# Kernel optimization log

Measured on AMD Instinct MI355X. Metric: run time of the kernel, lower is better.

The kernel has to match this reference:

```python
import jax, jax.numpy as jnp
import numpy as np

B, N, D = 8, 2048, 192
G, S = 512, 32
OUT = 384
ALPHA, BETA = 1000.0, 100.0
EPS = 1e-05


def setup_inputs() -> dict:
    key = jax.random.key(0)
    ks = jax.random.split(key, 8)
    sc = 0.02
    return {
        "points": jax.random.normal(ks[0], (B, N, 3), jnp.float32),
        "feats": jax.random.normal(ks[1], (B, N, D), jnp.float32),
        # 1x1 conv weights (BN assumed folded, inference form)
        "W1": sc * jax.random.normal(ks[2], (OUT, 2 * D), jnp.float32),
        "b1": jnp.zeros((OUT,), jnp.float32),
        "Wa": sc * jax.random.normal(ks[3], (OUT // 2, OUT), jnp.float32),
        "ba": jnp.zeros((OUT // 2,), jnp.float32),
        "Wb": sc * jax.random.normal(ks[4], (OUT, OUT // 2), jnp.float32),
        "bb": jnp.zeros((OUT,), jnp.float32),
    }


def fps(pts, n_samples):
    """Farthest point sampling. pts: (B,N,3) -> idx (B,n_samples) int32."""
    def one(p):  # (N,3)
        def step(carry, _):
            dists, last = carry
            cur = p[last]                                 # (3,)
            d = jnp.sum((p - cur) ** 2, axis=-1)          # (N,)
            dists = jnp.minimum(dists, d)
            nxt = jnp.argmax(dists).astype(jnp.int32)
            return (dists, nxt), last
        init = (jnp.full((p.shape[0],), jnp.inf, p.dtype), jnp.int32(0))
        _, idxs = jax.lax.scan(step, init, None, length=n_samples)
        return idxs
    return jax.vmap(one)(pts)


def pairwise_sqdist(a, b):
    # a: (B,G,3), b: (B,N,3) -> (B,G,N)
    aa = jnp.sum(a * a, -1)[:, :, None]
    bb = jnp.sum(b * b, -1)[:, None, :]
    return aa + bb - 2.0 * jnp.einsum('bgd,bnd->bgn', a, b)


def group_points(x, idx):
    # x: (B,N,C), idx: (B,G,S) -> (B,G,S,C)
    return jax.vmap(lambda f, i: f[i])(x, idx)


def pos_embed(xyz):
    # xyz: (B,G,S,3) -> (B,G,S,OUT)  Fourier positional encoding
    in_dim = xyz.shape[-1]
    feat_dim = OUT // (2 * in_dim)
    freq = jnp.arange(feat_dim, dtype=xyz.dtype)
    denom = jnp.power(jnp.asarray(ALPHA, xyz.dtype), freq / feat_dim)
    z = BETA * xyz[..., None] / denom                      # (B,G,S,3,feat_dim)
    pos = jnp.concatenate([jnp.sin(z), jnp.cos(z)], axis=-1)
    return pos.reshape(*xyz.shape[:-1], OUT)


def _forward(points, feats, W1, b1, Wa, ba, Wb, bb):
    # FPS centers
    fps_idx = fps(points, G)                               # (B,G)
    centers = jax.vmap(lambda p, i: p[i])(points, fps_idx)  # (B,G,3)

    d2 = pairwise_sqdist(centers, points)                  # (B,G,N)
    _, knn_idx = jax.lax.top_k(-d2, S)                     # (B,G,S)

    neighbor_pts = group_points(points, knn_idx)           # (B,G,S,3)
    neighbor_feats = group_points(feats, knn_idx)          # (B,G,S,D)

    # 'sim' normalization: global (scalar, unbiased) std of centered neighbors
    diff = neighbor_pts - centers[:, :, None, :]
    m = jnp.mean(diff)
    std = jnp.sqrt(jnp.sum((diff - m) ** 2) / (diff.size - 1))
    neighbor_pts = diff / (std + EPS)

    # center feats via 1-NN of centers in points
    center_idx = jnp.argmin(d2, axis=-1)                   # (B,G)
    center_feats = jax.vmap(lambda f, i: f[i])(feats, center_idx)  # (B,G,D)

    # concat neighbor + broadcast center feats -> (B,G,S,2D)
    gf = jnp.concatenate(
        [neighbor_feats, jnp.broadcast_to(center_feats[:, :, None, :], (points.shape[0], G, S, D))],
        axis=-1)

    # shared MLP (1x1 conv) + ReLU
    gf = jax.nn.relu(jnp.einsum('bgsc,oc->bgso', gf, W1) + b1)  # (B,G,S,OUT)

    pos = pos_embed(neighbor_pts)                          # (B,G,S,OUT)
    gf = (gf + pos) * pos

    # residual block: conv(OUT->OUT/2)+ReLU, conv(OUT/2->OUT), +x, ReLU
    h = jax.nn.relu(jnp.einsum('bgso,ho->bgsh', gf, Wa) + ba)
    h = jnp.einsum('bgsh,oh->bgso', h, Wb) + bb
    gf = jax.nn.relu(h + gf)

    # fused max + mean pooling over neighbors (S)
    out = jnp.max(gf, axis=2) + jnp.mean(gf, axis=2)       # (B,G,OUT)
    return centers, out


def reference(points, feats, W1, b1, Wa, ba, Wb, bb):
    return _forward(points, feats, W1, b1, Wa, ba, Wb, bb)
```

## Files before the change

kernel.cpp:

```cpp
#include <hip/hip_runtime.h>
#include <math.h>

#define Bn   8
#define Nn   2048
#define Dn   192
#define Gn   512
#define Sn   32
#define OUTn 384
#define Mrows (Bn * Gn * Sn)

typedef __attribute__((ext_vector_type(8))) unsigned short ushortx8;
typedef __attribute__((ext_vector_type(8))) __bf16 bf16x8;
typedef __attribute__((ext_vector_type(4))) float floatx4;

static constexpr size_t OFF_KNN   = 0;
static constexpr size_t OFF_CIDX  = 524288;
static constexpr size_t OFF_DIFF  = 540672;
static constexpr size_t OFF_SUMS  = 2113536;
static constexpr size_t OFF_STD   = 2113552;
static constexpr size_t OFF_DENOM = 2113792;
static constexpr size_t OFF_W1B   = 2114048;
static constexpr size_t OFF_WAB   = 2408960;
static constexpr size_t OFF_WBB   = 2556416;
static constexpr size_t OFF_G1    = 2703872;
static constexpr size_t OFF_FEATB = 103367168;

__device__ __forceinline__ unsigned short f2bf(float f) {
  unsigned u = __float_as_uint(f);
  unsigned r = (u + 0x7FFFu + ((u >> 16) & 1u)) >> 16;
  return (unsigned short)r;
}
__device__ __forceinline__ float bf2f(unsigned short h) {
  return __uint_as_float(((unsigned)h) << 16);
}
__device__ __forceinline__ floatx4 mfma_bf16(ushortx8 a, ushortx8 b, floatx4 c) {
  return __builtin_amdgcn_mfma_f32_16x16x32_bf16(
      __builtin_bit_cast(bf16x8, a), __builtin_bit_cast(bf16x8, b), c, 0, 0, 0);
}

__device__ __forceinline__ void gld16(const void* g, void* l) {
  __builtin_amdgcn_global_load_lds(
      (const __attribute__((address_space(1))) unsigned int*)g,
      (__attribute__((address_space(3))) unsigned int*)l, 16, 0, 0);
}

template <int CTRL>
__device__ __forceinline__ float dpp_max(float v) {
  int o = __builtin_amdgcn_update_dpp(0, __float_as_int(v), CTRL, 0xf, 0xf, true);
  return fmaxf(v, __int_as_float(o));
}

__global__ void prep_kernel(const float* __restrict__ W1, const float* __restrict__ Wa,
                            const float* __restrict__ Wb, const float* __restrict__ feats,
                            unsigned short* __restrict__ W1b, unsigned short* __restrict__ Wab,
                            unsigned short* __restrict__ Wbb, unsigned short* __restrict__ featb,
                            float* __restrict__ rdenomTab) {
  int i = blockIdx.x * 256 + threadIdx.x;
  if (i < 147456)            W1b[i] = f2bf(W1[i]);
  else if (i < 221184)       Wab[i - 147456] = f2bf(Wa[i - 147456]);
  else if (i < 294912)       Wbb[i - 221184] = f2bf(Wb[i - 221184]);
  else if (i < 3440640)      featb[i - 294912] = f2bf(feats[i - 294912]);
  if (blockIdx.x == 0 && threadIdx.x < 64)
    rdenomTab[threadIdx.x] = (float)(1.0 / pow(1000.0, (double)threadIdx.x / 64.0));
}

__global__ __launch_bounds__(256) void fps_kernel(const float* __restrict__ points,
                                                  float* __restrict__ centers) {
  const int b = blockIdx.x;
  const int t = threadIdx.x;
  const int w = t >> 6, lane = t & 63;
  __shared__ float4 p4[Nn];
  __shared__ unsigned long long wkey[2][4];

  const float* P = points + (size_t)b * Nn * 3;
  for (int n = t; n < Nn; n += 256) {
    float x = P[n * 3], y = P[n * 3 + 1], z = P[n * 3 + 2];
    p4[n] = make_float4(x, y, z, 0.f);
  }
  __syncthreads();

  float rx[8], ry[8], rz[8], dist[8];
#pragma unroll
  for (int k = 0; k < 8; ++k) {
    float4 p = p4[t * 8 + k];
    rx[k] = p.x; ry[k] = p.y; rz[k] = p.z;
    dist[k] = INFINITY;
  }

  int cur = 0;
  for (int it = 0; it < Gn; ++it) {
    const float4 c = p4[cur];
    if (t == 0) {
      float* cd = centers + ((size_t)b * Gn + it) * 3;
      cd[0] = c.x; cd[1] = c.y; cd[2] = c.z;
    }
    float bv = -1.0f;
#pragma unroll
    for (int k = 0; k < 8; ++k) {
      float dx = __fsub_rn(rx[k], c.x);
      float dy = __fsub_rn(ry[k], c.y);
      float dz = __fsub_rn(rz[k], c.z);
      float d = __fadd_rn(__fadd_rn(__fmul_rn(dx, dx), __fmul_rn(dy, dy)), __fmul_rn(dz, dz));
      dist[k] = fminf(dist[k], d);
      bv = fmaxf(bv, dist[k]);
    }
    int li = 7;
#pragma unroll
    for (int k = 6; k >= 0; --k) li = (dist[k] == bv) ? k : li;

    float red = bv;
    red = dpp_max<0x111>(red);
    red = dpp_max<0x112>(red);
    red = dpp_max<0x114>(red);
    red = dpp_max<0x118>(red);
    red = dpp_max<0x142>(red);
    red = dpp_max<0x143>(red);
    const float M = __int_as_float(__builtin_amdgcn_readlane(__float_as_int(red), 63));

    unsigned long long msk = __ballot(bv == M);
    const int L = __ffsll((long long)msk) - 1;
    const int liL = __builtin_amdgcn_readlane(li, L);
    const int idx = (w * 64 + L) * 8 + liL;

    unsigned long long key =
        ((unsigned long long)__float_as_uint(M) << 32) | (unsigned)(0x7FFFFFFF - idx);
    if (lane == 0) wkey[it & 1][w] = key;
    __syncthreads();
    unsigned long long k0 = wkey[it & 1][0];
    unsigned long long k1 = wkey[it & 1][1];
    unsigned long long k2 = wkey[it & 1][2];
    unsigned long long k3 = wkey[it & 1][3];
    unsigned long long m01 = (k1 > k0) ? k1 : k0;
    unsigned long long m23 = (k3 > k2) ? k3 : k2;
    unsigned long long mm = (m23 > m01) ? m23 : m01;
    cur = 0x7FFFFFFF - (int)(unsigned)mm;
  }
}

__global__ __launch_bounds__(256) void knn_kernel(const float* __restrict__ points,
                                                  const float* __restrict__ centers,
                                                  int* __restrict__ knn, int* __restrict__ cidx,
                                                  float* __restrict__ diffb,
                                                  double* __restrict__ sums) {
  const int t = threadIdx.x;
  const int w = t >> 6, lane = t & 63;
  const int bg = blockIdx.x * 4 + w;
  const int b = bg >> 9;

  const float* P = points + (size_t)b * Nn * 3;
  const float* cc = centers + (size_t)bg * 3;
  const float cx = cc[0], cy = cc[1], cz = cc[2];
  const float aa = __fadd_rn(__fadd_rn(__fmul_rn(cx, cx), __fmul_rn(cy, cy)), __fmul_rn(cz, cz));

  unsigned key[32];
#pragma unroll 8
  for (int s = 0; s < 32; ++s) {
    const int n = s * 64 + lane;
    float X = P[n * 3], Y = P[n * 3 + 1], Z = P[n * 3 + 2];
    float bbv = __fadd_rn(__fadd_rn(__fmul_rn(X, X), __fmul_rn(Y, Y)), __fmul_rn(Z, Z));
    float dot = __fadd_rn(__fadd_rn(__fmul_rn(cx, X), __fmul_rn(cy, Y)), __fmul_rn(cz, Z));
    float d2 = __fsub_rn(__fadd_rn(aa, bbv), __fmul_rn(2.0f, dot));
    unsigned u = __float_as_uint(d2);
    key[s] = u ^ ((unsigned)((int)u >> 31) | 0x80000000u);
  }

  unsigned mk = key[0]; int ms = 0;
#pragma unroll
  for (int s = 1; s < 32; ++s)
    if (key[s] < mk) { mk = key[s]; ms = s; }

  int mysel = 0;
  for (int it = 0; it < Sn; ++it) {
    unsigned long long p = ((unsigned long long)mk << 32) | (unsigned)(ms * 64 + lane);
#pragma unroll
    for (int off = 1; off <= 32; off <<= 1) {
      unsigned long long o = __shfl_xor(p, off, 64);
      p = (o < p) ? o : p;
    }
    const int n_win = (int)(unsigned)p;
    if (lane == it) mysel = n_win;
    if (lane == (n_win & 63)) {
      const int sw = n_win >> 6;
#pragma unroll
      for (int s = 0; s < 32; ++s)
        if (s == sw) key[s] = 0xFFFFFFFFu;
      mk = key[0]; ms = 0;
#pragma unroll
      for (int s = 1; s < 32; ++s)
        if (key[s] < mk) { mk = key[s]; ms = s; }
    }
  }

  double s1 = 0.0, s2 = 0.0;
  if (lane < Sn) {
    knn[(size_t)bg * Sn + lane] = mysel;
    float X = P[mysel * 3], Y = P[mysel * 3 + 1], Z = P[mysel * 3 + 2];
    float dx = __fsub_rn(X, cx), dy = __fsub_rn(Y, cy), dz = __fsub_rn(Z, cz);
    float* db = diffb + (size_t)bg * 96 + lane * 3;
    db[0] = dx; db[1] = dy; db[2] = dz;
    s1 = (double)dx + (double)dy + (double)dz;
    s2 = (double)dx * (double)dx + (double)dy * (double)dy + (double)dz * (double)dz;
  }
#pragma unroll
  for (int off = 1; off <= 32; off <<= 1) {
    s1 += __shfl_xor(s1, off, 64);
    s2 += __shfl_xor(s2, off, 64);
  }
  if (lane == 0) {
    cidx[bg] = __shfl(mysel, 0, 64);
    atomicAdd(sums, s1);
    atomicAdd(sums + 1, s2);
  }
}

__global__ void stddev_kernel(const double* __restrict__ sums, float* __restrict__ stdp) {
  const double n = (double)(Bn * Gn * Sn * 3);
  double s1 = sums[0], s2 = sums[1];
  double mean = s1 / n;
  double var = (s2 - s1 * mean) / (n - 1.0);
  float stdf = (float)sqrt(var) + 1e-5f;
  *stdp = (float)(1.0 / (double)stdf);
}

__global__ __launch_bounds__(256) void gemm1_kernel(
    const unsigned short* __restrict__ featb, const unsigned short* __restrict__ W1b,
    const float* __restrict__ b1, const int* __restrict__ knn,
    const int* __restrict__ cidx, const float* __restrict__ diffb,
    const float* __restrict__ rstd_p, const float* __restrict__ rdenomTab,
    unsigned short* __restrict__ G1) {
  __shared__ unsigned short As[128 * 64];
  __shared__ unsigned short Bs[128 * 64];
  const int t = threadIdx.x;
  const int bm = blockIdx.x, bn = blockIdx.y;
  const int wid = t >> 6, lane = t & 63, quad = lane >> 4, c16 = lane & 15;
  const int wr = wid >> 1, wc = wid & 1;

  int aOffN[4], aOffC[4], bOff[4];
#pragma unroll
  for (int i = 0; i < 4; ++i) {
    const int slot = i * 256 + t;
    const int row = slot >> 3, segV = slot & 7;
    const int seg = segV ^ (row & 7);
    const int grow = bm * 128 + row;
    const int bg = grow >> 5, s = grow & 31, bb_ = bg >> 9;
    const int nidx = knn[(size_t)bg * Sn + s];
    const int ci = cidx[bg];
    aOffN[i] = (bb_ * Nn + nidx) * Dn + seg * 8;
    aOffC[i] = (bb_ * Nn + ci) * Dn + seg * 8;
    bOff[i] = (bn * 128 + row) * 384 + seg * 8;
  }

  floatx4 acc[4][4];
#pragma unroll
  for (int i = 0; i < 4; ++i)
#pragma unroll
    for (int j = 0; j < 4; ++j) acc[i][j] = (floatx4){0.f, 0.f, 0.f, 0.f};

  for (int kt = 0; kt < 6; ++kt) {
    const int kb = kt * 64;
#pragma unroll
    for (int i = 0; i < 4; ++i) {
      const unsigned short* srcA =
          (kt < 3) ? (featb + aOffN[i] + kb) : (featb + aOffC[i] + (kb - 192));
      gld16(srcA, &As[(i * 256 + wid * 64) * 8]);
      gld16(W1b + bOff[i] + kb, &Bs[(i * 256 + wid * 64) * 8]);
    }
    __syncthreads();
#pragma unroll
    for (int ks = 0; ks < 2; ++ks) {
      ushortx8 af[4], bf[4];
#pragma unroll
      for (int mt = 0; mt < 4; ++mt) {
        const int row = wr * 64 + mt * 16 + c16;
        const int seg = (ks * 4 + quad) ^ (row & 7);
        af[mt] = *(const ushortx8*)&As[row * 64 + seg * 8];
      }
#pragma unroll
      for (int nt = 0; nt < 4; ++nt) {
        const int row = wc * 64 + nt * 16 + c16;
        const int seg = (ks * 4 + quad) ^ (row & 7);
        bf[nt] = *(const ushortx8*)&Bs[row * 64 + seg * 8];
      }
#pragma unroll
      for (int mt = 0; mt < 4; ++mt)
#pragma unroll
        for (int nt = 0; nt < 4; ++nt)
          acc[mt][nt] = mfma_bf16(af[mt], bf[nt], acc[mt][nt]);
    }
    __syncthreads();
  }

  const float rstd = *rstd_p;
  float bias[4], rdnm[4];
  bool usin[4];
#pragma unroll
  for (int nt = 0; nt < 4; ++nt) {
    const int col = bn * 128 + wc * 64 + nt * 16 + c16;
    bias[nt] = b1[col];
    const int j = col & 127;
    usin[nt] = (j < 64);
    rdnm[nt] = rdenomTab[j & 63];
  }
#pragma unroll
  for (int mt = 0; mt < 4; ++mt) {
#pragma unroll
    for (int r = 0; r < 4; ++r) {
      const int row = bm * 128 + wr * 64 + mt * 16 + quad * 4 + r;
      const float dv = diffb[(size_t)row * 3 + bn];
      const float x = __fmul_rn(dv, rstd);
      const float zb = __fmul_rn(100.0f, x);
#pragma unroll
      for (int nt = 0; nt < 4; ++nt) {
        const int col = bn * 128 + wc * 64 + nt * 16 + c16;
        float y = fmaxf(acc[mt][nt][r] + bias[nt], 0.f);
        float z = __fmul_rn(zb, rdnm[nt]);
        float p = usin[nt] ? __sinf(z) : __cosf(z);
        float g = (y + p) * p;
        G1[(size_t)row * 384 + col] = f2bf(g);
      }
    }
  }
}

__global__ __launch_bounds__(512) void gemm23_kernel(
    const unsigned short* __restrict__ G1, const unsigned short* __restrict__ Wab,
    const float* __restrict__ ba, const unsigned short* __restrict__ Wbb,
    const float* __restrict__ bb, float* __restrict__ outp) {
  __shared__ __align__(16) char smem[100352];
  unsigned short* Htile = (unsigned short*)smem;
  unsigned short* As    = (unsigned short*)(smem + 51200);
  unsigned short* BsA   = (unsigned short*)(smem + 51200 + 16384);
  unsigned short* BsB   = (unsigned short*)(smem + 51200);

  const int t = threadIdx.x;
  const int bm = blockIdx.x;
  const int lane = t & 63, quad = lane >> 4, c16 = lane & 15;
  const int wid = t >> 6;
  const int wr = wid >> 2, wc = wid & 3;

  int aOff[2], bOffA[3];
#pragma unroll
  for (int i = 0; i < 2; ++i) {
    const int slot = i * 512 + t;
    const int row = slot >> 3, segV = slot & 7;
    aOff[i] = (bm * 128 + row) * 384 + (segV ^ (row & 7)) * 8;
  }
#pragma unroll
  for (int i = 0; i < 3; ++i) {
    const int slot = i * 512 + t;
    const int row = slot >> 3, segV = slot & 7;
    bOffA[i] = row * 384 + (segV ^ (row & 7)) * 8;
  }

  floatx4 accA[4][3];
#pragma unroll
  for (int i = 0; i < 4; ++i)
#pragma unroll
    for (int j = 0; j < 3; ++j) accA[i][j] = (floatx4){0.f, 0.f, 0.f, 0.f};

  for (int kt = 0; kt < 6; ++kt) {
    const int kb = kt * 64;
#pragma unroll
    for (int i = 0; i < 2; ++i) gld16(G1 + aOff[i] + kb, As + ((size_t)(i * 512 + t)) * 8);
#pragma unroll
    for (int i = 0; i < 3; ++i) gld16(Wab + bOffA[i] + kb, BsA + ((size_t)(i * 512 + t)) * 8);
    __syncthreads();
#pragma unroll
    for (int ks = 0; ks < 2; ++ks) {
      ushortx8 af[4], bf[3];
#pragma unroll
      for (int mt = 0; mt < 4; ++mt) {
        const int row = wr * 64 + mt * 16 + c16;
        const int seg = (ks * 4 + quad) ^ (row & 7);
        af[mt] = *(const ushortx8*)&As[row * 64 + seg * 8];
      }
#pragma unroll
      for (int nt = 0; nt < 3; ++nt) {
        const int row = wc * 48 + nt * 16 + c16;
        const int seg = (ks * 4 + quad) ^ (row & 7);
        bf[nt] = *(const ushortx8*)&BsA[row * 64 + seg * 8];
      }
#pragma unroll
      for (int mt = 0; mt < 4; ++mt)
#pragma unroll
        for (int nt = 0; nt < 3; ++nt)
          accA[mt][nt] = mfma_bf16(af[mt], bf[nt], accA[mt][nt]);
    }
    __syncthreads();
  }

#pragma unroll
  for (int nt = 0; nt < 3; ++nt) {
    const int col = wc * 48 + nt * 16 + c16;
    const float bias = ba[col];
#pragma unroll
    for (int mt = 0; mt < 4; ++mt)
#pragma unroll
      for (int r = 0; r < 4; ++r) {
        const int row = wr * 64 + mt * 16 + quad * 4 + r;
        Htile[row * 200 + col] = f2bf(fmaxf(accA[mt][nt][r] + bias, 0.f));
      }
  }
  __syncthreads();

  int bOffB[6];
#pragma unroll
  for (int i = 0; i < 6; ++i) {
    const int slot = i * 512 + t;
    const int row = slot >> 3, segV = slot & 7;
    bOffB[i] = row * 192 + (segV ^ (row & 7)) * 8;
  }

  floatx4 acc[4][6];
#pragma unroll
  for (int i = 0; i < 4; ++i)
#pragma unroll
    for (int j = 0; j < 6; ++j) acc[i][j] = (floatx4){0.f, 0.f, 0.f, 0.f};

  for (int kt = 0; kt < 3; ++kt) {
    const int kb = kt * 64;
#pragma unroll
    for (int i = 0; i < 6; ++i) gld16(Wbb + bOffB[i] + kb, BsB + ((size_t)(i * 512 + t)) * 8);
    __syncthreads();
#pragma unroll
    for (int ks = 0; ks < 2; ++ks) {
      ushortx8 af[4], bf[6];
#pragma unroll
      for (int mt = 0; mt < 4; ++mt) {
        const int row = wr * 64 + mt * 16 + c16;
        af[mt] = *(const ushortx8*)&Htile[row * 200 + kb + ks * 32 + quad * 8];
      }
#pragma unroll
      for (int nt = 0; nt < 6; ++nt) {
        const int row = wc * 96 + nt * 16 + c16;
        const int seg = (ks * 4 + quad) ^ (row & 7);
        bf[nt] = *(const ushortx8*)&BsB[row * 64 + seg * 8];
      }
#pragma unroll
      for (int mt = 0; mt < 4; ++mt)
#pragma unroll
        for (int nt = 0; nt < 6; ++nt)
          acc[mt][nt] = mfma_bf16(af[mt], bf[nt], acc[mt][nt]);
    }
    __syncthreads();
  }

#pragma unroll
  for (int nt = 0; nt < 6; ++nt) {
    const int col = wc * 96 + nt * 16 + c16;
    const float bias = bb[col];
    float gmax[2] = {-INFINITY, -INFINITY};
    float gsum[2] = {0.f, 0.f};
#pragma unroll
    for (int mt = 0; mt < 4; ++mt) {
      const int grp = mt >> 1;
#pragma unroll
      for (int r = 0; r < 4; ++r) {
        const int row = bm * 128 + wr * 64 + mt * 16 + quad * 4 + r;
        float v = acc[mt][nt][r] + bias + bf2f(G1[(size_t)row * 384 + col]);
        v = fmaxf(v, 0.f);
        gmax[grp] = fmaxf(gmax[grp], v);
        gsum[grp] += v;
      }
    }
#pragma unroll
    for (int grp = 0; grp < 2; ++grp) {
      float m = gmax[grp], su = gsum[grp];
#pragma unroll
      for (int off = 16; off <= 32; off <<= 1) {
        m = fmaxf(m, __shfl_xor(m, off, 64));
        su += __shfl_xor(su, off, 64);
      }
      if (quad == 0) {
        const int bg = bm * 4 + wr * 2 + grp;
        outp[(size_t)bg * 384 + col] = m + su / 32.0f;
      }
    }
  }
}

extern "C" void kernel_launch(void* const* d_in, const int* in_sizes, int n_in,
                              void* d_out, int out_size, void* d_ws, size_t ws_size,
                              hipStream_t stream) {
  const float* points = (const float*)d_in[0];
  const float* feats  = (const float*)d_in[1];
  const float* W1 = (const float*)d_in[2];
  const float* b1 = (const float*)d_in[3];
  const float* Wa = (const float*)d_in[4];
  const float* ba = (const float*)d_in[5];
  const float* Wb = (const float*)d_in[6];
  const float* bb = (const float*)d_in[7];
  float* outF = (float*)d_out;

  char* ws = (char*)d_ws;
  int*            knn      = (int*)(ws + OFF_KNN);
  int*            cidx     = (int*)(ws + OFF_CIDX);
  float*          diffb    = (float*)(ws + OFF_DIFF);
  double*         sums     = (double*)(ws + OFF_SUMS);
  float*          stdp     = (float*)(ws + OFF_STD);
  float*          rdenomTab= (float*)(ws + OFF_DENOM);
  unsigned short* W1b      = (unsigned short*)(ws + OFF_W1B);
  unsigned short* Wab      = (unsigned short*)(ws + OFF_WAB);
  unsigned short* Wbb      = (unsigned short*)(ws + OFF_WBB);
  unsigned short* G1       = (unsigned short*)(ws + OFF_G1);
  unsigned short* featb    = (unsigned short*)(ws + OFF_FEATB);

  hipMemsetAsync(sums, 0, 2 * sizeof(double), stream);
  prep_kernel<<<13440, 256, 0, stream>>>(W1, Wa, Wb, feats, W1b, Wab, Wbb, featb, rdenomTab);
  fps_kernel<<<Bn, 256, 0, stream>>>(points, outF);
  knn_kernel<<<Bn * Gn / 4, 256, 0, stream>>>(points, outF, knn, cidx, diffb, sums);
  stddev_kernel<<<1, 1, 0, stream>>>(sums, stdp);
  gemm1_kernel<<<dim3(Mrows / 128, 3), 256, 0, stream>>>(featb, W1b, b1, knn, cidx,
                                                         diffb, stdp, rdenomTab, G1);
  gemm23_kernel<<<Mrows / 128, 512, 0, stream>>>(G1, Wab, ba, Wbb, bb, outF + Bn * Gn * 3);
}
```

Before: 556.6 us.

## Merge FPS with prep, fold stddev into KNN, retile gemm23 for occupancy

Several changes at once. The weight and feature bf16 conversion blocks now run in the same launch as the 8 FPS blocks, so the conversion overlaps the serial FPS loop. The stddev kernel is removed: the last KNN block, detected with an atomic counter, computes the reciprocal std itself. gemm23 moves from 128-row, 512-thread tiles to 64-row, 256-thread tiles with a smaller LDS footprint so two blocks can share a CU. In exchange each block reloads the full weights more often, and the larger per-wave accumulator arrays raise register pressure.

```diff
diff --git a/kernel.cpp b/kernel.cpp
--- a/kernel.cpp
+++ b/kernel.cpp
@@ -18,6 +18,7 @@
 static constexpr size_t OFF_DIFF  = 540672;
 static constexpr size_t OFF_SUMS  = 2113536;
 static constexpr size_t OFF_STD   = 2113552;
+static constexpr size_t OFF_CNT   = 2113568;
 static constexpr size_t OFF_DENOM = 2113792;
 static constexpr size_t OFF_W1B   = 2114048;
 static constexpr size_t OFF_WAB   = 2408960;
@@ -50,24 +51,31 @@
   return fmaxf(v, __int_as_float(o));
 }
 
-__global__ void prep_kernel(const float* __restrict__ W1, const float* __restrict__ Wa,
-                            const float* __restrict__ Wb, const float* __restrict__ feats,
-                            unsigned short* __restrict__ W1b, unsigned short* __restrict__ Wab,
-                            unsigned short* __restrict__ Wbb, unsigned short* __restrict__ featb,
-                            float* __restrict__ rdenomTab) {
-  int i = blockIdx.x * 256 + threadIdx.x;
-  if (i < 147456)            W1b[i] = f2bf(W1[i]);
-  else if (i < 221184)       Wab[i - 147456] = f2bf(Wa[i - 147456]);
-  else if (i < 294912)       Wbb[i - 221184] = f2bf(Wb[i - 221184]);
-  else if (i < 3440640)      featb[i - 294912] = f2bf(feats[i - 294912]);
-  if (blockIdx.x == 0 && threadIdx.x < 64)
-    rdenomTab[threadIdx.x] = (float)(1.0 / pow(1000.0, (double)threadIdx.x / 64.0));
-}
-
-__global__ __launch_bounds__(256) void fps_kernel(const float* __restrict__ points,
-                                                  float* __restrict__ centers) {
+__global__ __launch_bounds__(256) void fps_prep_kernel(
+    const float* __restrict__ points, float* __restrict__ centers,
+    const float* __restrict__ W1, const float* __restrict__ Wa,
+    const float* __restrict__ Wb, const float* __restrict__ feats,
+    unsigned short* __restrict__ W1b, unsigned short* __restrict__ Wab,
+    unsigned short* __restrict__ Wbb, unsigned short* __restrict__ featb,
+    float* __restrict__ rdenomTab) {
+  const int t = threadIdx.x;
+
+  if (blockIdx.x >= 8) {
+    const int base = (blockIdx.x - 8) * 1024 + t;
+#pragma unroll
+    for (int j = 0; j < 4; ++j) {
+      const int i = base + j * 256;
+      if (i < 147456)        W1b[i] = f2bf(W1[i]);
+      else if (i < 221184)   Wab[i - 147456] = f2bf(Wa[i - 147456]);
+      else if (i < 294912)   Wbb[i - 221184] = f2bf(Wb[i - 221184]);
+      else                   featb[i - 294912] = f2bf(feats[i - 294912]);
+    }
+    if (blockIdx.x == 8 && t < 64)
+      rdenomTab[t] = (float)(1.0 / pow(1000.0, (double)t / 64.0));
+    return;
+  }
+
   const int b = blockIdx.x;
-  const int t = threadIdx.x;
   const int w = t >> 6, lane = t & 63;
   __shared__ float4 p4[Nn];
   __shared__ unsigned long long wkey[2][4];
@@ -141,7 +149,9 @@
                                                   const float* __restrict__ centers,
                                                   int* __restrict__ knn, int* __restrict__ cidx,
                                                   float* __restrict__ diffb,
-                                                  double* __restrict__ sums) {
+                                                  double* __restrict__ sums,
+                                                  int* __restrict__ cnt,
+                                                  float* __restrict__ stdp) {
   const int t = threadIdx.x;
   const int w = t >> 6, lane = t & 63;
   const int bg = blockIdx.x * 4 + w;
@@ -211,15 +221,21 @@
     atomicAdd(sums, s1);
     atomicAdd(sums + 1, s2);
   }
-}
-
-__global__ void stddev_kernel(const double* __restrict__ sums, float* __restrict__ stdp) {
-  const double n = (double)(Bn * Gn * Sn * 3);
-  double s1 = sums[0], s2 = sums[1];
-  double mean = s1 / n;
-  double var = (s2 - s1 * mean) / (n - 1.0);
-  float stdf = (float)sqrt(var) + 1e-5f;
-  *stdp = (float)(1.0 / (double)stdf);
+  __threadfence();
+  __syncthreads();
+  if (t == 0) {
+    const int old = atomicAdd(cnt, 1);
+    if (old == (Bn * Gn / 4) - 1) {
+      __threadfence();
+      const double S1 = atomicAdd(sums, 0.0);
+      const double S2 = atomicAdd(sums + 1, 0.0);
+      const double n = (double)(Bn * Gn * Sn * 3);
+      const double mean = S1 / n;
+      const double var = (S2 - S1 * mean) / (n - 1.0);
+      const float stdf = (float)sqrt(var) + 1e-5f;
+      *stdp = (float)(1.0 / (double)stdf);
+    }
+  }
 }
 
 __global__ __launch_bounds__(256) void gemm1_kernel(
@@ -322,125 +338,69 @@
   }
 }
 
-__global__ __launch_bounds__(512) void gemm23_kernel(
+__global__ __launch_bounds__(256, 2) void gemm23_kernel(
     const unsigned short* __restrict__ G1, const unsigned short* __restrict__ Wab,
     const float* __restrict__ ba, const unsigned short* __restrict__ Wbb,
     const float* __restrict__ bb, float* __restrict__ outp) {
-  __shared__ __align__(16) char smem[100352];
+  __shared__ __align__(16) char smem[74752];
   unsigned short* Htile = (unsigned short*)smem;
-  unsigned short* As    = (unsigned short*)(smem + 51200);
-  unsigned short* BsA   = (unsigned short*)(smem + 51200 + 16384);
-  unsigned short* BsB   = (unsigned short*)(smem + 51200);
+  unsigned short* As    = (unsigned short*)(smem + 25600);
+  unsigned short* BsA   = (unsigned short*)(smem + 25600 + 8192);
+  unsigned short* BsB   = (unsigned short*)(smem + 25600);
 
   const int t = threadIdx.x;
   const int bm = blockIdx.x;
   const int lane = t & 63, quad = lane >> 4, c16 = lane & 15;
   const int wid = t >> 6;
-  const int wr = wid >> 2, wc = wid & 3;
-
-  int aOff[2], bOffA[3];
+  const int wr = wid >> 1, wc = wid & 1;
+
+  int aOff[2], bOffA[6];
 #pragma unroll
   for (int i = 0; i < 2; ++i) {
-    const int slot = i * 512 + t;
+    const int slot = i * 256 + t;
     const int row = slot >> 3, segV = slot & 7;
-    aOff[i] = (bm * 128 + row) * 384 + (segV ^ (row & 7)) * 8;
-  }
-#pragma unroll
-  for (int i = 0; i < 3; ++i) {
-    const int slot = i * 512 + t;
+    aOff[i] = (bm * 64 + row) * 384 + (segV ^ (row & 7)) * 8;
+  }
+#pragma unroll
+  for (int i = 0; i < 6; ++i) {
+    const int slot = i * 256 + t;
     const int row = slot >> 3, segV = slot & 7;
     bOffA[i] = row * 384 + (segV ^ (row & 7)) * 8;
   }
 
-  floatx4 accA[4][3];
-#pragma unroll
-  for (int i = 0; i < 4; ++i)
-#pragma unroll
-    for (int j = 0; j < 3; ++j) accA[i][j] = (floatx4){0.f, 0.f, 0.f, 0.f};
+  floatx4 accA[2][6];
+#pragma unroll
+  for (int i = 0; i < 2; ++i)
+#pragma unroll
+    for (int j = 0; j < 6; ++j) accA[i][j] = (floatx4){0.f, 0.f, 0.f, 0.f};
 
   for (int kt = 0; kt < 6; ++kt) {
     const int kb = kt * 64;
 #pragma unroll
-    for (int i = 0; i < 2; ++i) gld16(G1 + aOff[i] + kb, As + ((size_t)(i * 512 + t)) * 8);
-#pragma unroll
-    for (int i = 0; i < 3; ++i) gld16(Wab + bOffA[i] + kb, BsA + ((size_t)(i * 512 + t)) * 8);
+    for (int i = 0; i < 2; ++i) gld16(G1 + aOff[i] + kb, As + (size_t)(i * 256 + wid * 64) * 8);
+#pragma unroll
+    for (int i = 0; i < 6; ++i) gld16(Wab + bOffA[i] + kb, BsA + (size_t)(i * 256 + wid * 64) * 8);
     __syncthreads();
 #pragma unroll
     for (int ks = 0; ks < 2; ++ks) {
-      ushortx8 af[4], bf[3];
-#pragma unroll
-      for (int mt = 0; mt < 4; ++mt) {
-        const int row = wr * 64 + mt * 16 + c16;
+      ushortx8 af[2], bf[6];
+#pragma unroll
+      for (int mt = 0; mt < 2; ++mt) {
+        const int row = wr * 32 + mt * 16 + c16;
         const int seg = (ks * 4 + quad) ^ (row & 7);
         af[mt] = *(const ushortx8*)&As[row * 64 + seg * 8];
-      }
-#pragma unroll
-      for (int nt = 0; nt < 3; ++nt) {
-        const int row = wc * 48 + nt * 16 + c16;
-        const int seg = (ks * 4 + quad) ^ (row & 7);
-        bf[nt] = *(const ushortx8*)&BsA[row * 64 + seg * 8];
-      }
-#pragma unroll
-      for (int mt = 0; mt < 4; ++mt)
-#pragma unroll
-        for (int nt = 0; nt < 3; ++nt)
-          accA[mt][nt] = mfma_bf16(af[mt], bf[nt], accA[mt][nt]);
-    }
-    __syncthreads();
-  }
-
-#pragma unroll
-  for (int nt = 0; nt < 3; ++nt) {
-    const int col = wc * 48 + nt * 16 + c16;
-    const float bias = ba[col];
-#pragma unroll
-    for (int mt = 0; mt < 4; ++mt)
-#pragma unroll
-      for (int r = 0; r < 4; ++r) {
-        const int row = wr * 64 + mt * 16 + quad * 4 + r;
-        Htile[row * 200 + col] = f2bf(fmaxf(accA[mt][nt][r] + bias, 0.f));
-      }
-  }
-  __syncthreads();
-
-  int bOffB[6];
-#pragma unroll
-  for (int i = 0; i < 6; ++i) {
-    const int slot = i * 512 + t;
-    const int row = slot >> 3, segV = slot & 7;
-    bOffB[i] = row * 192 + (segV ^ (row & 7)) * 8;
-  }
-
-  floatx4 acc[4][6];
-#pragma unroll
-  for (int i = 0; i < 4; ++i)
-#pragma unroll
-    for (int j = 0; j < 6; ++j) acc[i][j] = (floatx4){0.f, 0.f, 0.f, 0.f};
-
-  for (int kt = 0; kt < 3; ++kt) {
-    const int kb = kt * 64;
-#pragma unroll
-    for (int i = 0; i < 6; ++i) gld16(Wbb + bOffB[i] + kb, BsB + ((size_t)(i * 512 + t)) * 8);
-    __syncthreads();
-#pragma unroll
-    for (int ks = 0; ks < 2; ++ks) {
-      ushortx8 af[4], bf[6];
-#pragma unroll
-      for (int mt = 0; mt < 4; ++mt) {
-        const int row = wr * 64 + mt * 16 + c16;
-        af[mt] = *(const ushortx8*)&Htile[row * 200 + kb + ks * 32 + quad * 8];
       }
 #pragma unroll
       for (int nt = 0; nt < 6; ++nt) {
         const int row = wc * 96 + nt * 16 + c16;
         const int seg = (ks * 4 + quad) ^ (row & 7);
-        bf[nt] = *(const ushortx8*)&BsB[row * 64 + seg * 8];
-      }
-#pragma unroll
-      for (int mt = 0; mt < 4; ++mt)
+        bf[nt] = *(const ushortx8*)&BsA[row * 64 + seg * 8];
+      }
+#pragma unroll
+      for (int mt = 0; mt < 2; ++mt)
 #pragma unroll
         for (int nt = 0; nt < 6; ++nt)
-          acc[mt][nt] = mfma_bf16(af[mt], bf[nt], acc[mt][nt]);
+          accA[mt][nt] = mfma_bf16(af[mt], bf[nt], accA[mt][nt]);
     }
     __syncthreads();
   }
@@ -448,33 +408,84 @@
 #pragma unroll
   for (int nt = 0; nt < 6; ++nt) {
     const int col = wc * 96 + nt * 16 + c16;
+    const float bias = ba[col];
+#pragma unroll
+    for (int mt = 0; mt < 2; ++mt)
+#pragma unroll
+      for (int r = 0; r < 4; ++r) {
+        const int row = wr * 32 + mt * 16 + quad * 4 + r;
+        Htile[row * 200 + col] = f2bf(fmaxf(accA[mt][nt][r] + bias, 0.f));
+      }
+  }
+  __syncthreads();
+
+  int bOffB[12];
+#pragma unroll
+  for (int i = 0; i < 12; ++i) {
+    const int slot = i * 256 + t;
+    const int row = slot >> 3, segV = slot & 7;
+    bOffB[i] = row * 192 + (segV ^ (row & 7)) * 8;
+  }
+
+  floatx4 acc[2][12];
+#pragma unroll
+  for (int i = 0; i < 2; ++i)
+#pragma unroll
+    for (int j = 0; j < 12; ++j) acc[i][j] = (floatx4){0.f, 0.f, 0.f, 0.f};
+
+  for (int kt = 0; kt < 3; ++kt) {
+    const int kb = kt * 64;
+#pragma unroll
+    for (int i = 0; i < 12; ++i)
+      gld16(Wbb + bOffB[i] + kb, BsB + (size_t)(i * 256 + wid * 64) * 8);
+    __syncthreads();
+#pragma unroll
+    for (int ks = 0; ks < 2; ++ks) {
+      ushortx8 af[2], bf[12];
+#pragma unroll
+      for (int mt = 0; mt < 2; ++mt) {
+        const int row = wr * 32 + mt * 16 + c16;
+        af[mt] = *(const ushortx8*)&Htile[row * 200 + kb + ks * 32 + quad * 8];
+      }
+#pragma unroll
+      for (int nt = 0; nt < 12; ++nt) {
+        const int row = wc * 192 + nt * 16 + c16;
+        const int seg = (ks * 4 + quad) ^ (row & 7);
+        bf[nt] = *(const ushortx8*)&BsB[row * 64 + seg * 8];
+      }
+#pragma unroll
+      for (int mt = 0; mt < 2; ++mt)
+#pragma unroll
+        for (int nt = 0; nt < 12; ++nt)
+          acc[mt][nt] = mfma_bf16(af[mt], bf[nt], acc[mt][nt]);
+    }
+    __syncthreads();
+  }
+
+#pragma unroll
+  for (int nt = 0; nt < 12; ++nt) {
+    const int col = wc * 192 + nt * 16 + c16;
     const float bias = bb[col];
-    float gmax[2] = {-INFINITY, -INFINITY};
-    float gsum[2] = {0.f, 0.f};
-#pragma unroll
-    for (int mt = 0; mt < 4; ++mt) {
-      const int grp = mt >> 1;
+    float gmax = -INFINITY, gsum = 0.f;
+#pragma unroll
+    for (int mt = 0; mt < 2; ++mt)
 #pragma unroll
       for (int r = 0; r < 4; ++r) {
-        const int row = bm * 128 + wr * 64 + mt * 16 + quad * 4 + r;
+        const int row = bm * 64 + wr * 32 + mt * 16 + quad * 4 + r;
         float v = acc[mt][nt][r] + bias + bf2f(G1[(size_t)row * 384 + col]);
         v = fmaxf(v, 0.f);
-        gmax[grp] = fmaxf(gmax[grp], v);
-        gsum[grp] += v;
-      }
-    }
-#pragma unroll
-    for (int grp = 0; grp < 2; ++grp) {
-      float m = gmax[grp], su = gsum[grp];
-#pragma unroll
-      for (int off = 16; off <= 32; off <<= 1) {
-        m = fmaxf(m, __shfl_xor(m, off, 64));
-        su += __shfl_xor(su, off, 64);
-      }
-      if (quad == 0) {
-        const int bg = bm * 4 + wr * 2 + grp;
-        outp[(size_t)bg * 384 + col] = m + su / 32.0f;
-      }
+        gmax = fmaxf(gmax, v);
+        gsum += v;
+      }
+    float m = gmax, su = gsum;
+#pragma unroll
+    for (int off = 16; off <= 32; off <<= 1) {
+      m = fmaxf(m, __shfl_xor(m, off, 64));
+      su += __shfl_xor(su, off, 64);
+    }
+    if (quad == 0) {
+      const int bg = bm * 2 + wr;
+      outp[(size_t)bg * 384 + col] = m + su / 32.0f;
     }
   }
 }
@@ -498,6 +509,7 @@
   float*          diffb    = (float*)(ws + OFF_DIFF);
   double*         sums     = (double*)(ws + OFF_SUMS);
   float*          stdp     = (float*)(ws + OFF_STD);
+  int*            cnt      = (int*)(ws + OFF_CNT);
   float*          rdenomTab= (float*)(ws + OFF_DENOM);
   unsigned short* W1b      = (unsigned short*)(ws + OFF_W1B);
   unsigned short* Wab      = (unsigned short*)(ws + OFF_WAB);
@@ -505,12 +517,12 @@
   unsigned short* G1       = (unsigned short*)(ws + OFF_G1);
   unsigned short* featb    = (unsigned short*)(ws + OFF_FEATB);
 
-  hipMemsetAsync(sums, 0, 2 * sizeof(double), stream);
-  prep_kernel<<<13440, 256, 0, stream>>>(W1, Wa, Wb, feats, W1b, Wab, Wbb, featb, rdenomTab);
-  fps_kernel<<<Bn, 256, 0, stream>>>(points, outF);
-  knn_kernel<<<Bn * Gn / 4, 256, 0, stream>>>(points, outF, knn, cidx, diffb, sums);
-  stddev_kernel<<<1, 1, 0, stream>>>(sums, stdp);
+  hipMemsetAsync(ws + OFF_SUMS, 0, 40, stream);
+  fps_prep_kernel<<<8 + 3360, 256, 0, stream>>>(points, outF, W1, Wa, Wb, feats,
+                                                W1b, Wab, Wbb, featb, rdenomTab);
+  knn_kernel<<<Bn * Gn / 4, 256, 0, stream>>>(points, outF, knn, cidx, diffb,
+                                              sums, cnt, stdp);
   gemm1_kernel<<<dim3(Mrows / 128, 3), 256, 0, stream>>>(featb, W1b, b1, knn, cidx,
                                                          diffb, stdp, rdenomTab, G1);
-  gemm23_kernel<<<Mrows / 128, 512, 0, stream>>>(G1, Wab, ba, Wbb, bb, outF + Bn * Gn * 3);
-}
+  gemm23_kernel<<<Mrows / 64, 256, 0, stream>>>(G1, Wab, ba, Wbb, bb, outF + Bn * Gn * 3);
+}
```

After: 573.4 us. 1.03x slower.
